# Kernel optimization log

Hardware: AMD Instinct MI355X
Metric: run time of the kernel (lower is better)

Reference implementation:

```python
import jax, jax.numpy as jnp
import numpy as np

C = 384; H = 32; W = 32; HEADS = 12; HD = C // HEADS; MLP = 1536
KOFF = 5; OFF_RANGE = 2.0


def layer_norm(x, g, b, eps=1e-5):
    mu = jnp.mean(x, axis=-1, keepdims=True)
    var = jnp.mean(jnp.square(x - mu), axis=-1, keepdims=True)
    return (x - mu) * jax.lax.rsqrt(var + eps) * g + b


def depthwise_conv(x, k):
    # x: (B,H,W,C), k: (kh,kw,1,C), SAME padding, groups=C
    return jax.lax.conv_general_dilated(
        x, k, window_strides=(1, 1), padding='SAME',
        dimension_numbers=('NHWC', 'HWIO', 'NHWC'), feature_group_count=C)


def grid_sample_bilinear(img, pos):
    # img: (B,H,W,C); pos: (B,H,W,2) normalized (y,x) in [-1,1], align_corners=True, border clamp
    B, Hh, Ww, Cc = img.shape
    py = (pos[..., 0] + 1.0) * 0.5 * (Hh - 1)
    px = (pos[..., 1] + 1.0) * 0.5 * (Ww - 1)
    y0 = jnp.floor(py); x0 = jnp.floor(px)
    wy = (py - y0)[..., None]; wx = (px - x0)[..., None]
    y0i = jnp.clip(y0.astype(jnp.int32), 0, Hh - 1)
    y1i = jnp.clip(y0i + 1, 0, Hh - 1)
    x0i = jnp.clip(x0.astype(jnp.int32), 0, Ww - 1)
    x1i = jnp.clip(x0i + 1, 0, Ww - 1)
    b = jnp.arange(B)[:, None, None]
    g = lambda yi, xi: img[b, yi, xi]
    return (g(y0i, x0i) * (1 - wy) * (1 - wx) + g(y0i, x1i) * (1 - wy) * wx
            + g(y1i, x0i) * wy * (1 - wx) + g(y1i, x1i) * wy * wx)


def setup_inputs() -> dict:
    key = jax.random.key(0)
    ks = jax.random.split(key, 16)
    n = jax.random.normal
    s = 0.02
    inp = {
        'x': n(ks[0], (16, H * W, C), jnp.float32),
        'ln1_g': jnp.ones((C,), jnp.float32), 'ln1_b': jnp.zeros((C,), jnp.float32),
        'Wq': n(ks[1], (C, C), jnp.float32) * s, 'bq': jnp.zeros((C,), jnp.float32),
        'off_k': n(ks[2], (KOFF, KOFF, 1, C), jnp.float32) * s,
        'off_kb': jnp.zeros((C,), jnp.float32),
        'offln_g': jnp.ones((C,), jnp.float32), 'offln_b': jnp.zeros((C,), jnp.float32),
        'Woff': n(ks[3], (2, C), jnp.float32) * s, 'boff': jnp.zeros((2,), jnp.float32),
        'Wk': n(ks[4], (C, C), jnp.float32) * s, 'bk': jnp.zeros((C,), jnp.float32),
        'Wv': n(ks[5], (C, C), jnp.float32) * s, 'bv': jnp.zeros((C,), jnp.float32),
        'Wo': n(ks[6], (C, C), jnp.float32) * s, 'bo': jnp.zeros((C,), jnp.float32),
        'ln2_g': jnp.ones((C,), jnp.float32), 'ln2_b': jnp.zeros((C,), jnp.float32),
        'W1': n(ks[7], (MLP, C), jnp.float32) * s, 'b1': jnp.zeros((MLP,), jnp.float32),
        'W2': n(ks[8], (C, MLP), jnp.float32) * s, 'b2': jnp.zeros((C,), jnp.float32),
    }
    return inp


def _block(x, ln1_g, ln1_b, Wq, bq, off_k, off_kb, offln_g, offln_b, Woff, boff,
           Wk, bk, Wv, bv, Wo, bo, ln2_g, ln2_b, W1, b1, W2, b2):
    B, N, _ = x.shape
    # --- deformable attention branch ---
    xn = layer_norm(x, ln1_g, ln1_b)
    xi = xn.reshape(B, H, W, C)
    q = xi @ Wq.T + bq                                  # (B,H,W,C)
    # offset network: depthwise conv -> LN -> GELU -> 1x1 conv to 2
    off = depthwise_conv(q, off_k) + off_kb
    off = jax.nn.gelu(layer_norm(off, offln_g, offln_b))
    off = off @ Woff.T + boff                           # (B,H,W,2)
    off_range = jnp.array([OFF_RANGE * 2.0 / H, OFF_RANGE * 2.0 / W], jnp.float32)
    off = jnp.tanh(off) * off_range                     # normalized coord units
    ry = (jnp.arange(H, dtype=jnp.float32) + 0.5) / H * 2.0 - 1.0
    rx = (jnp.arange(W, dtype=jnp.float32) + 0.5) / W * 2.0 - 1.0
    ref = jnp.stack(jnp.meshgrid(ry, rx, indexing='ij'), axis=-1)  # (H,W,2)
    pos = ref[None] + off                               # (B,H,W,2)
    xs = grid_sample_bilinear(xi, pos).reshape(B, N, C)  # sampled keys/values source
    k = xs @ Wk.T + bk
    v = xs @ Wv.T + bv
    qh = q.reshape(B, N, HEADS, HD).transpose(0, 2, 1, 3)
    kh = k.reshape(B, N, HEADS, HD).transpose(0, 2, 1, 3)
    vh = v.reshape(B, N, HEADS, HD).transpose(0, 2, 1, 3)
    attn = jax.nn.softmax(jnp.einsum('bhqd,bhkd->bhqk', qh, kh) * (HD ** -0.5), axis=-1)
    o = jnp.einsum('bhqk,bhkd->bhqd', attn, vh).transpose(0, 2, 1, 3).reshape(B, N, C)
    x = x + (o @ Wo.T + bo)
    # --- MLP branch ---
    y = layer_norm(x, ln2_g, ln2_b)
    y = jax.nn.gelu(y @ W1.T + b1) @ W2.T + b2
    return x + y


def reference(x, ln1_g, ln1_b, Wq, bq, off_k, off_kb, offln_g, offln_b, Woff, boff,
              Wk, bk, Wv, bv, Wo, bo, ln2_g, ln2_b, W1, b1, W2, b2):
    return _block(x, ln1_g, ln1_b, Wq, bq, off_k, off_kb, offln_g, offln_b, Woff, boff,
                  Wk, bk, Wv, bv, Wo, bo, ln2_g, ln2_b, W1, b1, W2, b2)
```

## Files before the change

### kernel.cpp

```cpp
#include <hip/hip_runtime.h>
#include <math.h>

#define DI __device__ __forceinline__

typedef __attribute__((ext_vector_type(8))) short bf16x8;
typedef __attribute__((ext_vector_type(4))) float f32x4;

static constexpr int CC = 384;
static constexpr float QSCALE = 0.17677669529663687f * 1.4426950408889634f;
static constexpr float INVQS  = 1.0f / QSCALE;

DI unsigned short f2bf(float f){
  unsigned u = __float_as_uint(f);
  u += 0x7FFFu + ((u >> 16) & 1u);
  return (unsigned short)(u >> 16);
}
DI float bf2f(unsigned short u){ return __uint_as_float((unsigned)u << 16); }
DI float lo16(unsigned u){ return __uint_as_float(u << 16); }
DI float hi16(unsigned u){ return __uint_as_float(u & 0xFFFF0000u); }
DI float fexp2(float x){ return __builtin_amdgcn_exp2f(x); }
DI float frcp(float x){ return __builtin_amdgcn_rcpf(x); }
DI float tanh_fast(float z){ return 1.f - 2.f*frcp(fexp2(2.8853900817779268f*z) + 1.f); }
DI float gelu_fast(float v){
  float u = v*v;
  float z = 0.7978845608028654f * fmaf(0.044715f*u, v, v);
  return v - v*frcp(fexp2(2.8853900817779268f*z) + 1.f);
}
DI f32x4 mfma16(bf16x8 a, bf16x8 b, f32x4 c){
  return __builtin_amdgcn_mfma_f32_16x16x32_bf16(a, b, c, 0, 0, 0);
}
DI void gload16(const unsigned short* g, unsigned short* l){
  __builtin_amdgcn_global_load_lds(
      (const __attribute__((address_space(1))) unsigned int*)(const void*)g,
      (__attribute__((address_space(3))) unsigned int*)(void*)l, 16, 0, 0);
}
DI unsigned packbf(float pa, float pb){
  return __builtin_amdgcn_perm(__float_as_uint(pb), __float_as_uint(pa), 0x07060302u);
}

__global__ __launch_bounds__(256) void k_cvt_all(
    const float* __restrict__ wq, const float* __restrict__ wk,
    const float* __restrict__ wv, const float* __restrict__ wo,
    const float* __restrict__ w1, const float* __restrict__ w2,
    const float* __restrict__ ofk,
    unsigned short* __restrict__ dst)
{
  int i4 = (blockIdx.x*256 + threadIdx.x)*4;
  if (i4 >= 1779072) return;
  const float* src; int off;
  if (i4 < 147456){ src = wq; off = i4; }
  else if (i4 < 294912){ src = wk; off = i4 - 147456; }
  else if (i4 < 442368){ src = wv; off = i4 - 294912; }
  else if (i4 < 589824){ src = wo; off = i4 - 442368; }
  else if (i4 < 1179648){ src = w1; off = i4 - 589824; }
  else if (i4 < 1769472){ src = w2; off = i4 - 1179648; }
  else { src = ofk; off = i4 - 1769472; }
  float4 v = *(const float4*)(src + off);
  uint2 o;
  o.x = ((unsigned)f2bf(v.y) << 16) | f2bf(v.x);
  o.y = ((unsigned)f2bf(v.w) << 16) | f2bf(v.z);
  *(uint2*)(dst + i4) = o;
}

template<int BIN>
__global__ __launch_bounds__(256) void k_ln(const float* __restrict__ xf,
    const unsigned short* __restrict__ xb,
    const float* __restrict__ g, const float* __restrict__ b,
    unsigned short* __restrict__ outb, unsigned short* __restrict__ outb2)
{
  int row = blockIdx.x*4 + (threadIdx.x >> 6);
  int l = threadIdx.x & 63;
  float v[6]; int ch[6];
  if constexpr (BIN){
    int cA = 4*l, cB = 256 + 2*l;
    ch[0]=cA; ch[1]=cA+1; ch[2]=cA+2; ch[3]=cA+3; ch[4]=cB; ch[5]=cB+1;
    const unsigned short* xp = xb + (size_t)row * CC;
    uint2 u2 = *(const uint2*)(xp + cA);
    unsigned u1 = *(const unsigned*)(xp + cB);
    v[0]=lo16(u2.x); v[1]=hi16(u2.x); v[2]=lo16(u2.y); v[3]=hi16(u2.y);
    v[4]=lo16(u1);   v[5]=hi16(u1);
  } else {
    const float* xp = xf + (size_t)row * CC;
#pragma unroll
    for (int p = 0; p < 6; p++){ ch[p] = l + 64*p; v[p] = xp[ch[p]]; }
  }
  float s = 0.f, s2 = 0.f;
#pragma unroll
  for (int p = 0; p < 6; p++){ s += v[p]; s2 += v[p]*v[p]; }
#pragma unroll
  for (int m = 32; m; m >>= 1){ s += __shfl_xor(s, m); s2 += __shfl_xor(s2, m); }
  float mu = s * (1.f/CC);
  float var = s2 * (1.f/CC) - mu*mu;
  float rs = rsqrtf(var + 1e-5f);
  float o[6];
#pragma unroll
  for (int p = 0; p < 6; p++) o[p] = (v[p] - mu) * rs * g[ch[p]] + b[ch[p]];
  unsigned short* op = outb + (size_t)row*CC;
  if constexpr (BIN){
    uint2 st;
    st.x = ((unsigned)f2bf(o[1]) << 16) | f2bf(o[0]);
    st.y = ((unsigned)f2bf(o[3]) << 16) | f2bf(o[2]);
    *(uint2*)(op + ch[0]) = st;
    *(unsigned*)(op + ch[4]) = ((unsigned)f2bf(o[5]) << 16) | f2bf(o[4]);
  } else {
#pragma unroll
    for (int p = 0; p < 6; p++) op[ch[p]] = f2bf(o[p]);
    if (outb2){
      unsigned short* op2 = outb2 + (size_t)row*CC;
#pragma unroll
      for (int p = 0; p < 6; p++) op2[ch[p]] = f2bf(v[p]);
    }
  }
}

template<int EPI>
__global__ __launch_bounds__(256) void k_g64(
    const unsigned short* __restrict__ A, const unsigned short* __restrict__ W,
    const float* __restrict__ bias, const float* __restrict__ bias2,
    const unsigned short* __restrict__ resb,
    float* __restrict__ outf, unsigned short* __restrict__ outb,
    unsigned short* __restrict__ outb2, int ntn, int N, int K)
{
  __shared__ unsigned short As[2][4096];
  __shared__ unsigned short Bs[2][8192];
  int bid = blockIdx.x;
  int cpx = gridDim.x >> 3;
  int id = (bid & 7)*cpx + (bid >> 3);
  int bn = (id % ntn) * 128;
  int bm = (id / ntn) * 64;
  int t = threadIdx.x;
  int w = t >> 6, l = t & 63;
  int g = l >> 4, ln = l & 15;
  int wm = w >> 1, wn = w & 1;
  f32x4 acc[2][4];
#pragma unroll
  for (int i = 0; i < 2; i++)
#pragma unroll
    for (int j = 0; j < 4; j++) acc[i][j] = (f32x4){0.f,0.f,0.f,0.f};
  int srcoff = ((t & 7) ^ ((t >> 3) & 7)) * 8;
  int srowA = t >> 3;
  const unsigned short* Ap0 = A + (size_t)(bm + srowA)*K + srcoff;
  const unsigned short* Ap1 = A + (size_t)(bm + 32 + srowA)*K + srcoff;
  const unsigned short* Wp0 = W + (size_t)(bn + srowA)*K + srcoff;
  const unsigned short* Wp1 = W + (size_t)(bn + 32 + srowA)*K + srcoff;
  const unsigned short* Wp2 = W + (size_t)(bn + 64 + srowA)*K + srcoff;
  const unsigned short* Wp3 = W + (size_t)(bn + 96 + srowA)*K + srcoff;
  int NT = K >> 6;
  int wl = w*512;
  gload16(Ap0, &As[0][wl]);
  gload16(Ap1, &As[0][wl + 2048]);
  gload16(Wp0, &Bs[0][wl]);
  gload16(Wp1, &Bs[0][wl + 2048]);
  gload16(Wp2, &Bs[0][wl + 4096]);
  gload16(Wp3, &Bs[0][wl + 6144]);
  __syncthreads();
  for (int kt = 0; kt < NT; kt++){
    int cur = kt & 1;
    if (kt + 1 < NT){
      int k0 = (kt + 1) << 6;
      gload16(Ap0 + k0, &As[cur ^ 1][wl]);
      gload16(Ap1 + k0, &As[cur ^ 1][wl + 2048]);
      gload16(Wp0 + k0, &Bs[cur ^ 1][wl]);
      gload16(Wp1 + k0, &Bs[cur ^ 1][wl + 2048]);
      gload16(Wp2 + k0, &Bs[cur ^ 1][wl + 4096]);
      gload16(Wp3 + k0, &Bs[cur ^ 1][wl + 6144]);
    }
#pragma unroll
    for (int kk = 0; kk < 2; kk++){
      bf16x8 af[2], bf[4];
#pragma unroll
      for (int mi = 0; mi < 2; mi++){
        int row = wm*32 + mi*16 + ln;
        int sl = (kk*4 + g) ^ (row & 7);
        af[mi] = *(const bf16x8*)((const char*)As[cur] + row*128 + sl*16);
      }
#pragma unroll
      for (int ni = 0; ni < 4; ni++){
        int row = wn*64 + ni*16 + ln;
        int sl = (kk*4 + g) ^ (row & 7);
        bf[ni] = *(const bf16x8*)((const char*)Bs[cur] + row*128 + sl*16);
      }
#pragma unroll
      for (int mi = 0; mi < 2; mi++)
#pragma unroll
        for (int ni = 0; ni < 4; ni++)
          acc[mi][ni] = mfma16(af[mi], bf[ni], acc[mi][ni]);
    }
    if (kt + 1 < NT) __syncthreads();
  }
#pragma unroll
  for (int mi = 0; mi < 2; mi++)
#pragma unroll
  for (int ni = 0; ni < 4; ni++){
    int col = bn + wn*64 + ni*16 + ln;
    float bv;
    if constexpr (EPI == 6) bv = col < 384 ? bias[col] : bias2[col - 384];
    else bv = bias[col];
#pragma unroll
    for (int i = 0; i < 4; i++){
      int row = bm + wm*32 + mi*16 + g*4 + i;
      float v = acc[mi][ni][i] + bv;
      if constexpr (EPI == 5) outb[(size_t)row*N + col] = f2bf(v * QSCALE);
      if constexpr (EPI == 7){ v += bf2f(resb[(size_t)row*N + col]); outf[(size_t)row*N + col] = v; }
      if constexpr (EPI == 8){ v += bf2f(resb[(size_t)row*N + col]); outb[(size_t)row*N + col] = f2bf(v); }
      if constexpr (EPI == 6){
        if (col < 384){
          outb[(size_t)row*384 + col] = f2bf(v);
        } else {
          int c = col - 384;
          int bb = row >> 10, key = row & 1023, h = c >> 5, d = c & 31;
          int k6 = key & 63;
          int phys = (key & ~63) | (k6 & 0x23) | ((k6 & 0xC) << 1) | ((k6 & 0x10) >> 2);
          outb2[(size_t)(((bb*12 + h) << 5) + d)*1024 + phys] = f2bf(v);
        }
      }
    }
  }
}

__global__ __launch_bounds__(256) void k_mlp1(
    const unsigned short* __restrict__ A, const unsigned short* __restrict__ W,
    const float* __restrict__ bias, unsigned short* __restrict__ outb)
{
  __shared__ unsigned short As[2][4096];
  __shared__ unsigned short Bs[2][4096];
  int bid = blockIdx.x;
  int cpx = gridDim.x >> 3;
  int id = (bid & 7)*cpx + (bid >> 3);
  int bn = (id % 12) * 128;
  int bm = (id / 12) * 128;
  int t = threadIdx.x;
  int w = t >> 6, l = t & 63;
  int g = l >> 4, ln = l & 15;
  int wm = w >> 1, wn = w & 1;
  f32x4 acc[4][4];
#pragma unroll
  for (int i = 0; i < 4; i++)
#pragma unroll
    for (int j = 0; j < 4; j++) acc[i][j] = (f32x4){0.f,0.f,0.f,0.f};
  int srow0 = t >> 2, slot = t & 3;
  int srow1 = srow0 + 64;
  int cb0 = (slot ^ (srow0 & 3) ^ ((srow0 >> 2) & 3)) * 8;
  int cb1 = (slot ^ (srow1 & 3) ^ ((srow1 >> 2) & 3)) * 8;
  const unsigned short* Ap0 = A + (size_t)(bm + srow0)*384 + cb0;
  const unsigned short* Ap1 = A + (size_t)(bm + srow1)*384 + cb1;
  const unsigned short* Wp0 = W + (size_t)(bn + srow0)*384 + cb0;
  const unsigned short* Wp1 = W + (size_t)(bn + srow1)*384 + cb1;
  int wl = w*512;
  gload16(Ap0, &As[0][wl]);
  gload16(Ap1, &As[0][wl + 2048]);
  gload16(Wp0, &Bs[0][wl]);
  gload16(Wp1, &Bs[0][wl + 2048]);
  __syncthreads();
  for (int kt = 0; kt < 12; kt++){
    int cur = kt & 1;
    if (kt < 11){
      int k0 = (kt + 1) << 5;
      gload16(Ap0 + k0, &As[cur ^ 1][wl]);
      gload16(Ap1 + k0, &As[cur ^ 1][wl + 2048]);
      gload16(Wp0 + k0, &Bs[cur ^ 1][wl]);
      gload16(Wp1 + k0, &Bs[cur ^ 1][wl + 2048]);
    }
    bf16x8 af[4], bf[4];
#pragma unroll
    for (int mi = 0; mi < 4; mi++){
      int row = wm*64 + mi*16 + ln;
      int sl = g ^ (row & 3) ^ ((row >> 2) & 3);
      af[mi] = *(const bf16x8*)((const char*)As[cur] + row*64 + sl*16);
    }
#pragma unroll
    for (int ni = 0; ni < 4; ni++){
      int row = wn*64 + ni*16 + ln;
      int sl = g ^ (row & 3) ^ ((row >> 2) & 3);
      bf[ni] = *(const bf16x8*)((const char*)Bs[cur] + row*64 + sl*16);
    }
#pragma unroll
    for (int mi = 0; mi < 4; mi++)
#pragma unroll
      for (int ni = 0; ni < 4; ni++)
        acc[mi][ni] = mfma16(af[mi], bf[ni], acc[mi][ni]);
    if (kt < 11) __syncthreads();
  }
#pragma unroll
  for (int mi = 0; mi < 4; mi++)
#pragma unroll
  for (int ni = 0; ni < 4; ni++){
    int col = bn + wn*64 + ni*16 + ln;
    float bv = bias[col];
#pragma unroll
    for (int i = 0; i < 4; i++){
      int row = bm + wm*64 + mi*16 + g*4 + i;
      float v = gelu_fast(acc[mi][ni][i] + bv);
      outb[(size_t)row*1536 + col] = f2bf(v);
    }
  }
}

__global__ __launch_bounds__(64) void k_offset_sample(
    const unsigned short* __restrict__ qs, const unsigned short* __restrict__ xnb,
    const unsigned short* __restrict__ okb,
    const float* __restrict__ offkb,
    const float* __restrict__ offg, const float* __restrict__ offb,
    const float* __restrict__ Woff, const float* __restrict__ boff,
    unsigned short* __restrict__ xsb)
{
  int blk = blockIdx.x;
  int pix = (blk & 7)*2048 + (blk >> 3);
  int b = pix >> 10, n = pix & 1023;
  int y = n >> 5, x = n & 31;
  int t = threadIdx.x;
  int c8 = (t < 48 ? t : 47) * 8;
  float act = t < 48 ? 1.f : 0.f;
  const unsigned short* qb = qs + (size_t)b*1024*CC;
  int ry[5], rx[5]; unsigned my[5], mx[5];
#pragma unroll
  for (int k = 0; k < 5; k++){
    int yy = y + k - 2, xx = x + k - 2;
    my[k] = (yy >= 0 && yy < 32) ? 0xFFFFFFFFu : 0u;
    mx[k] = (xx >= 0 && xx < 32) ? 0xFFFFFFFFu : 0u;
    int yc = yy < 0 ? 0 : (yy > 31 ? 31 : yy);
    int xc = xx < 0 ? 0 : (xx > 31 ? 31 : xx);
    ry[k] = yc*32*CC; rx[k] = xc*CC;
  }
  float a[8];
#pragma unroll
  for (int j = 0; j < 8; j++) a[j] = 0.f;
#pragma unroll
  for (int ky = 0; ky < 5; ky++)
#pragma unroll
  for (int kx = 0; kx < 5; kx++){
    int tap = ky*5 + kx;
    unsigned m = my[ky] & mx[kx];
    uint4 q4 = *(const uint4*)(qb + ry[ky] + rx[kx] + c8);
    uint4 w4 = *(const uint4*)(okb + tap*CC + c8);
    q4.x &= m; q4.y &= m; q4.z &= m; q4.w &= m;
    a[0] = fmaf(lo16(q4.x), lo16(w4.x), a[0]);
    a[1] = fmaf(hi16(q4.x), hi16(w4.x), a[1]);
    a[2] = fmaf(lo16(q4.y), lo16(w4.y), a[2]);
    a[3] = fmaf(hi16(q4.y), hi16(w4.y), a[3]);
    a[4] = fmaf(lo16(q4.z), lo16(w4.z), a[4]);
    a[5] = fmaf(hi16(q4.z), hi16(w4.z), a[5]);
    a[6] = fmaf(lo16(q4.w), lo16(w4.w), a[6]);
    a[7] = fmaf(hi16(q4.w), hi16(w4.w), a[7]);
  }
  float4 kbA = *(const float4*)(offkb + c8);
  float4 kbB = *(const float4*)(offkb + c8 + 4);
  float c[8];
  c[0] = act * fmaf(a[0], INVQS, kbA.x);
  c[1] = act * fmaf(a[1], INVQS, kbA.y);
  c[2] = act * fmaf(a[2], INVQS, kbA.z);
  c[3] = act * fmaf(a[3], INVQS, kbA.w);
  c[4] = act * fmaf(a[4], INVQS, kbB.x);
  c[5] = act * fmaf(a[5], INVQS, kbB.y);
  c[6] = act * fmaf(a[6], INVQS, kbB.z);
  c[7] = act * fmaf(a[7], INVQS, kbB.w);
  float s = 0.f, s2 = 0.f;
#pragma unroll
  for (int j = 0; j < 8; j++){ s += c[j]; s2 += c[j]*c[j]; }
#pragma unroll
  for (int m2 = 32; m2; m2 >>= 1){ s += __shfl_xor(s, m2); s2 += __shfl_xor(s2, m2); }
  float mu = s * (1.f/CC);
  float var = s2 * (1.f/CC) - mu*mu;
  float rs = rsqrtf(var + 1e-5f);
  float4 gA = *(const float4*)(offg + c8); float4 gB = *(const float4*)(offg + c8 + 4);
  float4 oA = *(const float4*)(offb + c8); float4 oB = *(const float4*)(offb + c8 + 4);
  float4 wA = *(const float4*)(Woff + c8); float4 wB = *(const float4*)(Woff + c8 + 4);
  float4 wC = *(const float4*)(Woff + CC + c8); float4 wD = *(const float4*)(Woff + CC + c8 + 4);
  float gg[8] = {gA.x,gA.y,gA.z,gA.w,gB.x,gB.y,gB.z,gB.w};
  float bb[8] = {oA.x,oA.y,oA.z,oA.w,oB.x,oB.y,oB.z,oB.w};
  float w0[8] = {wA.x,wA.y,wA.z,wA.w,wB.x,wB.y,wB.z,wB.w};
  float w1[8] = {wC.x,wC.y,wC.z,wC.w,wD.x,wD.y,wD.z,wD.w};
  float p0 = 0.f, p1 = 0.f;
#pragma unroll
  for (int j = 0; j < 8; j++){
    float v = gelu_fast((c[j] - mu)*rs*gg[j] + bb[j]) * act;
    p0 = fmaf(v, w0[j], p0);
    p1 = fmaf(v, w1[j], p1);
  }
#pragma unroll
  for (int m2 = 32; m2; m2 >>= 1){ p0 += __shfl_xor(p0, m2); p1 += __shfl_xor(p1, m2); }
  float offy = tanh_fast(p0 + boff[0]) * 0.125f;
  float offx = tanh_fast(p1 + boff[1]) * 0.125f;
  float py = ((y + 0.5f)/16.f - 1.f + offy + 1.f) * 0.5f * 31.f;
  float px = ((x + 0.5f)/16.f - 1.f + offx + 1.f) * 0.5f * 31.f;
  float y0f = floorf(py), x0f = floorf(px);
  float wy = py - y0f, wx = px - x0f;
  int y0 = (int)y0f, x0 = (int)x0f;
  y0 = y0 < 0 ? 0 : (y0 > 31 ? 31 : y0);
  x0 = x0 < 0 ? 0 : (x0 > 31 ? 31 : x0);
  int y1 = y0 + 1 > 31 ? 31 : y0 + 1;
  int x1 = x0 + 1 > 31 ? 31 : x0 + 1;
  const unsigned short* s00 = xnb + (size_t)(b*1024 + y0*32 + x0)*CC + c8;
  const unsigned short* s01 = xnb + (size_t)(b*1024 + y0*32 + x1)*CC + c8;
  const unsigned short* s10 = xnb + (size_t)(b*1024 + y1*32 + x0)*CC + c8;
  const unsigned short* s11 = xnb + (size_t)(b*1024 + y1*32 + x1)*CC + c8;
  float w00 = (1.f-wy)*(1.f-wx), w01 = (1.f-wy)*wx, w10 = wy*(1.f-wx), w11 = wy*wx;
  uint4 A0 = *(const uint4*)s00;
  uint4 A1 = *(const uint4*)s01;
  uint4 A2 = *(const uint4*)s10;
  uint4 A3 = *(const uint4*)s11;
  if (t < 48){
    float r[8];
    r[0] = w00*lo16(A0.x) + w01*lo16(A1.x) + w10*lo16(A2.x) + w11*lo16(A3.x);
    r[1] = w00*hi16(A0.x) + w01*hi16(A1.x) + w10*hi16(A2.x) + w11*hi16(A3.x);
    r[2] = w00*lo16(A0.y) + w01*lo16(A1.y) + w10*lo16(A2.y) + w11*lo16(A3.y);
    r[3] = w00*hi16(A0.y) + w01*hi16(A1.y) + w10*hi16(A2.y) + w11*hi16(A3.y);
    r[4] = w00*lo16(A0.z) + w01*lo16(A1.z) + w10*lo16(A2.z) + w11*lo16(A3.z);
    r[5] = w00*hi16(A0.z) + w01*hi16(A1.z) + w10*hi16(A2.z) + w11*hi16(A3.z);
    r[6] = w00*lo16(A0.w) + w01*lo16(A1.w) + w10*lo16(A2.w) + w11*lo16(A3.w);
    r[7] = w00*hi16(A0.w) + w01*hi16(A1.w) + w10*hi16(A2.w) + w11*hi16(A3.w);
    uint4 st;
    st.x = ((unsigned)f2bf(r[1]) << 16) | f2bf(r[0]);
    st.y = ((unsigned)f2bf(r[3]) << 16) | f2bf(r[2]);
    st.z = ((unsigned)f2bf(r[5]) << 16) | f2bf(r[4]);
    st.w = ((unsigned)f2bf(r[7]) << 16) | f2bf(r[6]);
    *(uint4*)(xsb + (size_t)(b*1024 + n)*CC + c8) = st;
  }
}

__global__ __launch_bounds__(256) void k_attn(
    const unsigned short* __restrict__ qs, const unsigned short* __restrict__ kb,
    const unsigned short* __restrict__ vt, unsigned short* __restrict__ ob)
{
  __shared__ unsigned short Ks[2][64][40];
  __shared__ unsigned short Vs[2][32][72];
  int blk = blockIdx.x;
  int sw = (blk & 7)*96 + (blk >> 3);
  int qt = sw & 3, h = (sw >> 2) % 12, b = sw / 48;
  int t = threadIdx.x;
  int w = t >> 6, l = t & 63;
  int g = l >> 4, ln = l & 15;
  int q0 = qt*256 + w*64;
  bf16x8 qa[4];
#pragma unroll
  for (int mi = 0; mi < 4; mi++)
    qa[mi] = *(const bf16x8*)&qs[(size_t)(b*1024 + q0 + mi*16 + ln)*CC + h*32 + g*8];
  bf16x8 vones;
#pragma unroll
  for (int j = 0; j < 8; j++) vones[j] = (short)0x3F80;
  f32x4 z = {0.f,0.f,0.f,0.f};
  f32x4 oacc[4][2];
#pragma unroll
  for (int mi = 0; mi < 4; mi++){ oacc[mi][0]=z; oacc[mi][1]=z; }
  f32x4 lacc[4]; lacc[0]=z; lacc[1]=z; lacc[2]=z; lacc[3]=z;
  int krow = t >> 2, kc = (t & 3)*8;
  int vdim = t >> 3, vc = (t & 7)*8;
  const unsigned short* kptr = kb + (size_t)(b*1024 + krow)*CC + h*32 + kc;
  const unsigned short* vptr = vt + (size_t)((b*12 + h)*32 + vdim)*1024 + vc;
  {
    uint4 kr = *(const uint4*)kptr;
    uint4 vr = *(const uint4*)vptr;
    *(uint4*)&Ks[0][krow][kc] = kr;
    *(uint4*)&Vs[0][vdim][vc] = vr;
  }
  __syncthreads();
  for (int kt = 0; kt < 16; kt++){
    int cur = kt & 1;
    uint4 kr2, vr2;
    if (kt < 15){
      int k0 = (kt + 1)*64;
      kr2 = *(const uint4*)(kptr + (size_t)k0*CC);
      vr2 = *(const uint4*)(vptr + k0);
    }
#pragma unroll
    for (int k2 = 0; k2 < 2; k2++){
      bf16x8 kf0 = *(const bf16x8*)&Ks[cur][(2*k2)*16 + ln][g*8];
      bf16x8 kf1 = *(const bf16x8*)&Ks[cur][(2*k2+1)*16 + ln][g*8];
      bf16x8 va0 = *(const bf16x8*)&Vs[cur][ln][k2*32 + g*8];
      bf16x8 va1 = *(const bf16x8*)&Vs[cur][16 + ln][k2*32 + g*8];
      __builtin_amdgcn_s_setprio(1);
#pragma unroll
      for (int mi = 0; mi < 4; mi++){
        f32x4 s0 = mfma16(kf0, qa[mi], z);
        f32x4 s1 = mfma16(kf1, qa[mi], z);
        float e0 = fexp2(s0[0]), e1 = fexp2(s0[1]);
        float e2 = fexp2(s0[2]), e3 = fexp2(s0[3]);
        float f0 = fexp2(s1[0]), f1 = fexp2(s1[1]);
        float f2 = fexp2(s1[2]), f3 = fexp2(s1[3]);
        uint4 pw;
        pw.x = packbf(e0, e1);
        pw.y = packbf(e2, e3);
        pw.z = packbf(f0, f1);
        pw.w = packbf(f2, f3);
        bf16x8 pa = *(bf16x8*)&pw;
        oacc[mi][0] = mfma16(pa, va0, oacc[mi][0]);
        oacc[mi][1] = mfma16(pa, va1, oacc[mi][1]);
        lacc[mi] = mfma16(pa, vones, lacc[mi]);
      }
      __builtin_amdgcn_s_setprio(0);
    }
    if (kt < 15){
      *(uint4*)&Ks[cur ^ 1][krow][kc] = kr2;
      *(uint4*)&Vs[cur ^ 1][vdim][vc] = vr2;
      __syncthreads();
    }
  }
  float rinv[4][4];
#pragma unroll
  for (int mi = 0; mi < 4; mi++)
#pragma unroll
    for (int i = 0; i < 4; i++) rinv[mi][i] = frcp(lacc[mi][i]);
#pragma unroll
  for (int mi = 0; mi < 4; mi++)
#pragma unroll
  for (int d2 = 0; d2 < 2; d2++)
#pragma unroll
  for (int i = 0; i < 4; i++){
    float v = oacc[mi][d2][i] * rinv[mi][i];
    int row = q0 + mi*16 + g*4 + i;
    ob[(size_t)(b*1024 + row)*CC + h*32 + d2*16 + ln] = f2bf(v);
  }
}

extern "C" void kernel_launch(void* const* d_in, const int* in_sizes, int n_in,
                              void* d_out, int out_size, void* d_ws, size_t ws_size,
                              hipStream_t stream)
{
  (void)in_sizes; (void)n_in; (void)out_size; (void)ws_size;
  const float* x     = (const float*)d_in[0];
  const float* ln1g  = (const float*)d_in[1];
  const float* ln1b  = (const float*)d_in[2];
  const float* Wq    = (const float*)d_in[3];
  const float* bq    = (const float*)d_in[4];
  const float* offk  = (const float*)d_in[5];
  const float* offkb = (const float*)d_in[6];
  const float* offg  = (const float*)d_in[7];
  const float* offb  = (const float*)d_in[8];
  const float* Woff  = (const float*)d_in[9];
  const float* boff  = (const float*)d_in[10];
  const float* Wk    = (const float*)d_in[11];
  const float* bk    = (const float*)d_in[12];
  const float* Wv    = (const float*)d_in[13];
  const float* bv    = (const float*)d_in[14];
  const float* Wo    = (const float*)d_in[15];
  const float* bo    = (const float*)d_in[16];
  const float* ln2g  = (const float*)d_in[17];
  const float* ln2b  = (const float*)d_in[18];
  const float* W1    = (const float*)d_in[19];
  const float* b1    = (const float*)d_in[20];
  const float* W2    = (const float*)d_in[21];
  const float* b2    = (const float*)d_in[22];

  char* ws = (char*)d_ws;
  unsigned short* X2B = (unsigned short*)ws;
  unsigned short* XB  = (unsigned short*)(ws + 12582912);
  unsigned short* XSB = (unsigned short*)(ws + 25165824);
  unsigned short* KB  = (unsigned short*)(ws + 37748736);
  unsigned short* VT  = (unsigned short*)(ws + 50331648);
  unsigned short* OB  = (unsigned short*)(ws + 62914560);
  unsigned short* XNB = (unsigned short*)(ws + 75497472);
  unsigned short* QSB = (unsigned short*)(ws + 88080384);
  unsigned short* YB  = QSB;
  unsigned short* HB  = (unsigned short*)(ws + 25165824);
  unsigned short* WQB = (unsigned short*)(ws + 100663296);
  unsigned short* WKB = WQB + 147456;
  unsigned short* WOB = WKB + 294912;
  unsigned short* W1B = WOB + 147456;
  unsigned short* W2B = W1B + 589824;
  unsigned short* OKB = W2B + 589824;

  k_cvt_all<<<1738, 256, 0, stream>>>(Wq, Wk, Wv, Wo, W1, W2, offk, WQB);
  k_ln<0><<<4096, 256, 0, stream>>>(x, nullptr, ln1g, ln1b, XNB, XB);
  k_g64<5><<<768, 256, 0, stream>>>(XNB, WQB, bq, nullptr, nullptr, nullptr, QSB, nullptr, 3, 384, 384);
  k_offset_sample<<<16384, 64, 0, stream>>>(QSB, XNB, OKB, offkb, offg, offb, Woff, boff, XSB);
  k_g64<6><<<1536, 256, 0, stream>>>(XSB, WKB, bk, bv, nullptr, nullptr, KB, VT, 6, 768, 384);
  k_attn<<<768, 256, 0, stream>>>(QSB, KB, VT, OB);
  k_g64<8><<<768, 256, 0, stream>>>(OB, WOB, bo, nullptr, XB, nullptr, X2B, nullptr, 3, 384, 384);
  k_ln<1><<<4096, 256, 0, stream>>>(nullptr, X2B, ln2g, ln2b, YB, nullptr);
  k_mlp1<<<1536, 256, 0, stream>>>(YB, W1B, b1, HB);
  k_g64<7><<<768, 256, 0, stream>>>(HB, W2B, b2, nullptr, X2B, (float*)d_out, nullptr, nullptr, 3, 384, 1536);
}
```

Baseline: 210.0 us.

## Double attention key tile to 128 and route MLP1 through generic 64-row GEMM

The attention kernel now stages 128 keys per shared-memory tile instead of 64, halving the number of loop iterations and barriers while doubling LDS usage per block. Separately, the dedicated 128x128 MLP1 GEMM kernel is removed and replaced with the generic k_g64 kernel using a new GELU epilogue, launched with twice as many smaller blocks. This trades per-block data reuse for more parallelism, and adds register and LDS pressure in attention.

```diff
diff --git a/kernel.cpp b/kernel.cpp
--- a/kernel.cpp
+++ b/kernel.cpp
@@ -200,6 +200,7 @@
     for (int i = 0; i < 4; i++){
       int row = bm + wm*32 + mi*16 + g*4 + i;
       float v = acc[mi][ni][i] + bv;
+      if constexpr (EPI == 3) outb[(size_t)row*N + col] = f2bf(gelu_fast(v));
       if constexpr (EPI == 5) outb[(size_t)row*N + col] = f2bf(v * QSCALE);
       if constexpr (EPI == 7){ v += bf2f(resb[(size_t)row*N + col]); outf[(size_t)row*N + col] = v; }
       if constexpr (EPI == 8){ v += bf2f(resb[(size_t)row*N + col]); outb[(size_t)row*N + col] = f2bf(v); }
@@ -214,84 +215,6 @@
           outb2[(size_t)(((bb*12 + h) << 5) + d)*1024 + phys] = f2bf(v);
         }
       }
-    }
-  }
-}
-
-__global__ __launch_bounds__(256) void k_mlp1(
-    const unsigned short* __restrict__ A, const unsigned short* __restrict__ W,
-    const float* __restrict__ bias, unsigned short* __restrict__ outb)
-{
-  __shared__ unsigned short As[2][4096];
-  __shared__ unsigned short Bs[2][4096];
-  int bid = blockIdx.x;
-  int cpx = gridDim.x >> 3;
-  int id = (bid & 7)*cpx + (bid >> 3);
-  int bn = (id % 12) * 128;
-  int bm = (id / 12) * 128;
-  int t = threadIdx.x;
-  int w = t >> 6, l = t & 63;
-  int g = l >> 4, ln = l & 15;
-  int wm = w >> 1, wn = w & 1;
-  f32x4 acc[4][4];
-#pragma unroll
-  for (int i = 0; i < 4; i++)
-#pragma unroll
-    for (int j = 0; j < 4; j++) acc[i][j] = (f32x4){0.f,0.f,0.f,0.f};
-  int srow0 = t >> 2, slot = t & 3;
-  int srow1 = srow0 + 64;
-  int cb0 = (slot ^ (srow0 & 3) ^ ((srow0 >> 2) & 3)) * 8;
-  int cb1 = (slot ^ (srow1 & 3) ^ ((srow1 >> 2) & 3)) * 8;
-  const unsigned short* Ap0 = A + (size_t)(bm + srow0)*384 + cb0;
-  const unsigned short* Ap1 = A + (size_t)(bm + srow1)*384 + cb1;
-  const unsigned short* Wp0 = W + (size_t)(bn + srow0)*384 + cb0;
-  const unsigned short* Wp1 = W + (size_t)(bn + srow1)*384 + cb1;
-  int wl = w*512;
-  gload16(Ap0, &As[0][wl]);
-  gload16(Ap1, &As[0][wl + 2048]);
-  gload16(Wp0, &Bs[0][wl]);
-  gload16(Wp1, &Bs[0][wl + 2048]);
-  __syncthreads();
-  for (int kt = 0; kt < 12; kt++){
-    int cur = kt & 1;
-    if (kt < 11){
-      int k0 = (kt + 1) << 5;
-      gload16(Ap0 + k0, &As[cur ^ 1][wl]);
-      gload16(Ap1 + k0, &As[cur ^ 1][wl + 2048]);
-      gload16(Wp0 + k0, &Bs[cur ^ 1][wl]);
-      gload16(Wp1 + k0, &Bs[cur ^ 1][wl + 2048]);
-    }
-    bf16x8 af[4], bf[4];
-#pragma unroll
-    for (int mi = 0; mi < 4; mi++){
-      int row = wm*64 + mi*16 + ln;
-      int sl = g ^ (row & 3) ^ ((row >> 2) & 3);
-      af[mi] = *(const bf16x8*)((const char*)As[cur] + row*64 + sl*16);
-    }
-#pragma unroll
-    for (int ni = 0; ni < 4; ni++){
-      int row = wn*64 + ni*16 + ln;
-      int sl = g ^ (row & 3) ^ ((row >> 2) & 3);
-      bf[ni] = *(const bf16x8*)((const char*)Bs[cur] + row*64 + sl*16);
-    }
-#pragma unroll
-    for (int mi = 0; mi < 4; mi++)
-#pragma unroll
-      for (int ni = 0; ni < 4; ni++)
-        acc[mi][ni] = mfma16(af[mi], bf[ni], acc[mi][ni]);
-    if (kt < 11) __syncthreads();
-  }
-#pragma unroll
-  for (int mi = 0; mi < 4; mi++)
-#pragma unroll
-  for (int ni = 0; ni < 4; ni++){
-    int col = bn + wn*64 + ni*16 + ln;
-    float bv = bias[col];
-#pragma unroll
-    for (int i = 0; i < 4; i++){
-      int row = bm + wm*64 + mi*16 + g*4 + i;
-      float v = gelu_fast(acc[mi][ni][i] + bv);
-      outb[(size_t)row*1536 + col] = f2bf(v);
     }
   }
 }
@@ -422,8 +345,8 @@
     const unsigned short* __restrict__ qs, const unsigned short* __restrict__ kb,
     const unsigned short* __restrict__ vt, unsigned short* __restrict__ ob)
 {
-  __shared__ unsigned short Ks[2][64][40];
-  __shared__ unsigned short Vs[2][32][72];
+  __shared__ unsigned short Ks[2][128][40];
+  __shared__ unsigned short Vs[2][32][136];
   int blk = blockIdx.x;
   int sw = (blk & 7)*96 + (blk >> 3);
   int qt = sw & 3, h = (sw >> 2) % 12, b = sw / 48;
@@ -448,50 +371,61 @@
   const unsigned short* kptr = kb + (size_t)(b*1024 + krow)*CC + h*32 + kc;
   const unsigned short* vptr = vt + (size_t)((b*12 + h)*32 + vdim)*1024 + vc;
   {
-    uint4 kr = *(const uint4*)kptr;
-    uint4 vr = *(const uint4*)vptr;
-    *(uint4*)&Ks[0][krow][kc] = kr;
-    *(uint4*)&Vs[0][vdim][vc] = vr;
+    uint4 k0r = *(const uint4*)kptr;
+    uint4 k1r = *(const uint4*)(kptr + (size_t)64*CC);
+    uint4 v0r = *(const uint4*)vptr;
+    uint4 v1r = *(const uint4*)(vptr + 64);
+    *(uint4*)&Ks[0][krow][kc] = k0r;
+    *(uint4*)&Ks[0][64 + krow][kc] = k1r;
+    *(uint4*)&Vs[0][vdim][vc] = v0r;
+    *(uint4*)&Vs[0][vdim][64 + vc] = v1r;
   }
   __syncthreads();
-  for (int kt = 0; kt < 16; kt++){
+  for (int kt = 0; kt < 8; kt++){
     int cur = kt & 1;
-    uint4 kr2, vr2;
-    if (kt < 15){
-      int k0 = (kt + 1)*64;
-      kr2 = *(const uint4*)(kptr + (size_t)k0*CC);
-      vr2 = *(const uint4*)(vptr + k0);
-    }
-#pragma unroll
-    for (int k2 = 0; k2 < 2; k2++){
-      bf16x8 kf0 = *(const bf16x8*)&Ks[cur][(2*k2)*16 + ln][g*8];
-      bf16x8 kf1 = *(const bf16x8*)&Ks[cur][(2*k2+1)*16 + ln][g*8];
-      bf16x8 va0 = *(const bf16x8*)&Vs[cur][ln][k2*32 + g*8];
-      bf16x8 va1 = *(const bf16x8*)&Vs[cur][16 + ln][k2*32 + g*8];
-      __builtin_amdgcn_s_setprio(1);
-#pragma unroll
-      for (int mi = 0; mi < 4; mi++){
-        f32x4 s0 = mfma16(kf0, qa[mi], z);
-        f32x4 s1 = mfma16(kf1, qa[mi], z);
-        float e0 = fexp2(s0[0]), e1 = fexp2(s0[1]);
-        float e2 = fexp2(s0[2]), e3 = fexp2(s0[3]);
-        float f0 = fexp2(s1[0]), f1 = fexp2(s1[1]);
-        float f2 = fexp2(s1[2]), f3 = fexp2(s1[3]);
-        uint4 pw;
-        pw.x = packbf(e0, e1);
-        pw.y = packbf(e2, e3);
-        pw.z = packbf(f0, f1);
-        pw.w = packbf(f2, f3);
-        bf16x8 pa = *(bf16x8*)&pw;
-        oacc[mi][0] = mfma16(pa, va0, oacc[mi][0]);
-        oacc[mi][1] = mfma16(pa, va1, oacc[mi][1]);
-        lacc[mi] = mfma16(pa, vones, lacc[mi]);
+    uint4 k0r, k1r, v0r, v1r;
+    if (kt < 7){
+      size_t k0 = (size_t)(kt + 1)*128;
+      k0r = *(const uint4*)(kptr + k0*CC);
+      k1r = *(const uint4*)(kptr + (k0 + 64)*CC);
+      v0r = *(const uint4*)(vptr + k0);
+      v1r = *(const uint4*)(vptr + k0 + 64);
+    }
+#pragma unroll
+    for (int sub = 0; sub < 2; sub++){
+#pragma unroll
+      for (int k2 = 0; k2 < 2; k2++){
+        bf16x8 kf0 = *(const bf16x8*)&Ks[cur][sub*64 + (2*k2)*16 + ln][g*8];
+        bf16x8 kf1 = *(const bf16x8*)&Ks[cur][sub*64 + (2*k2+1)*16 + ln][g*8];
+        bf16x8 va0 = *(const bf16x8*)&Vs[cur][ln][sub*64 + k2*32 + g*8];
+        bf16x8 va1 = *(const bf16x8*)&Vs[cur][16 + ln][sub*64 + k2*32 + g*8];
+        __builtin_amdgcn_s_setprio(1);
+#pragma unroll
+        for (int mi = 0; mi < 4; mi++){
+          f32x4 s0 = mfma16(kf0, qa[mi], z);
+          f32x4 s1 = mfma16(kf1, qa[mi], z);
+          float e0 = fexp2(s0[0]), e1 = fexp2(s0[1]);
+          float e2 = fexp2(s0[2]), e3 = fexp2(s0[3]);
+          float f0 = fexp2(s1[0]), f1 = fexp2(s1[1]);
+          float f2 = fexp2(s1[2]), f3 = fexp2(s1[3]);
+          uint4 pw;
+          pw.x = packbf(e0, e1);
+          pw.y = packbf(e2, e3);
+          pw.z = packbf(f0, f1);
+          pw.w = packbf(f2, f3);
+          bf16x8 pa = *(bf16x8*)&pw;
+          oacc[mi][0] = mfma16(pa, va0, oacc[mi][0]);
+          oacc[mi][1] = mfma16(pa, va1, oacc[mi][1]);
+          lacc[mi] = mfma16(pa, vones, lacc[mi]);
+        }
+        __builtin_amdgcn_s_setprio(0);
       }
-      __builtin_amdgcn_s_setprio(0);
-    }
-    if (kt < 15){
-      *(uint4*)&Ks[cur ^ 1][krow][kc] = kr2;
-      *(uint4*)&Vs[cur ^ 1][vdim][vc] = vr2;
+    }
+    if (kt < 7){
+      *(uint4*)&Ks[cur ^ 1][krow][kc] = k0r;
+      *(uint4*)&Ks[cur ^ 1][64 + krow][kc] = k1r;
+      *(uint4*)&Vs[cur ^ 1][vdim][vc] = v0r;
+      *(uint4*)&Vs[cur ^ 1][vdim][64 + vc] = v1r;
       __syncthreads();
     }
   }
@@ -567,6 +501,6 @@
   k_attn<<<768, 256, 0, stream>>>(QSB, KB, VT, OB);
   k_g64<8><<<768, 256, 0, stream>>>(OB, WOB, bo, nullptr, XB, nullptr, X2B, nullptr, 3, 384, 384);
   k_ln<1><<<4096, 256, 0, stream>>>(nullptr, X2B, ln2g, ln2b, YB, nullptr);
-  k_mlp1<<<1536, 256, 0, stream>>>(YB, W1B, b1, HB);
+  k_g64<3><<<3072, 256, 0, stream>>>(YB, W1B, b1, nullptr, nullptr, nullptr, HB, nullptr, 12, 1536, 384);
   k_g64<7><<<768, 256, 0, stream>>>(HB, W2B, b2, nullptr, X2B, (float*)d_out, nullptr, nullptr, 3, 384, 1536);
 }
```

After: 208.1 us. About the same (-0.9%).
